# Performance work log

Measured on AMD Instinct MI355X. Metric: run time of the kernel, lower is better.

The kernel has to match this reference:

```python
import jax, jax.numpy as jnp
import numpy as np

S, B, D, H, FF, L, V, O = 512, 32, 512, 8, 2048, 6, 32000, 1000
DH = D // H
EPS = 1e-5


def layer_norm(x, g, b):
    mu = jnp.mean(x, axis=-1, keepdims=True)
    var = jnp.mean((x - mu) ** 2, axis=-1, keepdims=True)
    return (x - mu) * jax.lax.rsqrt(var + EPS) * g + b


def positional_encoding(seq_len, dim):
    pos = np.arange(seq_len, dtype=np.float32)[:, None]
    i = np.arange(dim)
    angle = pos / (10000.0 ** ((i // 2 * 2.0) / dim))
    pe = np.where(i % 2 == 0, np.sin(angle), np.cos(angle)).astype(np.float32)
    return jnp.asarray(pe)  # [seq_len, dim]


def setup_inputs() -> dict:
    key = jax.random.key(0)
    ks = jax.random.split(key, 16)
    sc = 0.02
    inp = {
        'x': jax.random.randint(ks[0], (S, B), 0, V, dtype=jnp.int32),
        'x_len': jnp.full((B,), S, dtype=jnp.int32),
        'emb': jax.random.normal(ks[1], (V, D), jnp.float32) * sc,
        'Wq': jax.random.normal(ks[2], (L, D, D), jnp.float32) * sc,
        'bq': jnp.zeros((L, D), jnp.float32),
        'Wk': jax.random.normal(ks[3], (L, D, D), jnp.float32) * sc,
        'bk': jnp.zeros((L, D), jnp.float32),
        'Wv': jax.random.normal(ks[4], (L, D, D), jnp.float32) * sc,
        'bv': jnp.zeros((L, D), jnp.float32),
        'Wo': jax.random.normal(ks[5], (L, D, D), jnp.float32) * sc,
        'bo': jnp.zeros((L, D), jnp.float32),
        'ln1_g': jnp.ones((L, D), jnp.float32),
        'ln1_b': jnp.zeros((L, D), jnp.float32),
        'W1': jax.random.normal(ks[6], (L, D, FF), jnp.float32) * sc,
        'b1': jnp.zeros((L, FF), jnp.float32),
        'W2': jax.random.normal(ks[7], (L, FF, D), jnp.float32) * sc,
        'b2': jnp.zeros((L, D), jnp.float32),
        'ln2_g': jnp.ones((L, D), jnp.float32),
        'ln2_b': jnp.zeros((L, D), jnp.float32),
        'W_fc': jax.random.normal(ks[8], (S * D, O), jnp.float32) * sc,
        'b_fc': jnp.zeros((O,), jnp.float32),
    }
    return inp


def reference(x, x_len, emb, Wq, bq, Wk, bk, Wv, bv, Wo, bo, ln1_g, ln1_b,
              W1, b1, W2, b2, ln2_g, ln2_b, W_fc, b_fc):
    out = emb[x]                      # [S, B, D]
    out = jnp.transpose(out, (1, 0, 2))  # [B, S, D]
    out = out + positional_encoding(S, D)[None, :, :]
    scale = DH ** -0.5
    for l in range(L):
        # NOTE: faithful to the original buggy head-split: plain row-major
        # reshape [B,S,D] -> [B*H,S,DH] without a [B,H,S,DH] transpose.
        q = jnp.reshape(out @ Wq[l] + bq[l], (B * H, S, DH))
        k = jnp.reshape(out @ Wk[l] + bk[l], (B * H, S, DH))
        v = jnp.reshape(out @ Wv[l] + bv[l], (B * H, S, DH))
        attn = jax.nn.softmax(jnp.einsum('gqd,gkd->gqk', q, k) * scale, axis=-1)
        ctx = jnp.einsum('gqk,gkd->gqd', attn, v).reshape(B, S, D)
        h = layer_norm(ctx @ Wo[l] + bo[l] + out, ln1_g[l], ln1_b[l])
        f = jax.nn.relu(h @ W1[l] + b1[l]) @ W2[l] + b2[l]
        out = layer_norm(f + h, ln2_g[l], ln2_b[l])
    out = out.reshape(B, S * D)
    return out @ W_fc + b_fc          # [B, O]
```

## Files before the change

kernel.cpp:

```cpp
#include <hip/hip_runtime.h>
#include <cstdint>
#include <cstddef>

#define S_  512
#define B_  32
#define D_  512
#define FF_ 2048
#define L_  6
#define O_  1000
#define M_  (B_*S_)
#define G_  256
#define DH_ 64

typedef __attribute__((ext_vector_type(8))) short bf16x8;
typedef __attribute__((ext_vector_type(4))) float f32x4;
typedef __attribute__((ext_vector_type(16))) float f32x16;

__device__ __forceinline__ unsigned short f2bf(float f) {
  unsigned int u = __builtin_bit_cast(unsigned int, f);
  u = (u + 0x7fffu + ((u >> 16) & 1u)) >> 16;
  return (unsigned short)u;
}
__device__ __forceinline__ float bf2f(unsigned short u) {
  return __builtin_bit_cast(float, (unsigned int)u << 16);
}
__device__ __forceinline__ unsigned int pkbf(float a, float b) {
  return (unsigned int)f2bf(a) | ((unsigned int)f2bf(b) << 16);
}
__device__ __forceinline__ void gload_lds16(const void* g, void* l) {
  __builtin_amdgcn_global_load_lds(
      (const __attribute__((address_space(1))) unsigned int*)g,
      (__attribute__((address_space(3))) unsigned int*)l, 16, 0, 0);
}

__global__ void pe_kernel(float* __restrict__ pe) {
  int i = blockIdx.x * 256 + threadIdx.x;
  int s = i >> 9, d = i & 511;
  double de = (double)(d & ~1);
  double ang = (double)s * exp(de * (-9.210340371976184 / 512.0));
  pe[i] = (d & 1) ? (float)cos(ang) : (float)sin(ang);
}

__global__ void wconv_kernel(const float* __restrict__ W, unsigned short* __restrict__ Wt,
                             int K, int N, size_t ozs) {
  __shared__ float tile[32][33];
  const float* Wl = W + (size_t)blockIdx.z * K * N;
  unsigned short* Wtl = Wt + (size_t)blockIdx.z * ozs;
  int k0 = blockIdx.x * 32, n0 = blockIdx.y * 32;
  int c = threadIdx.x & 31, rb = threadIdx.x >> 5;
#pragma unroll
  for (int i = 0; i < 4; ++i) {
    int r = rb + i * 8;
    tile[r][c] = Wl[(size_t)(k0 + r) * N + n0 + c];
  }
  __syncthreads();
#pragma unroll
  for (int i = 0; i < 4; ++i) {
    int r = rb + i * 8;
    Wtl[(size_t)(n0 + r) * K + k0 + c] = f2bf(tile[c][r]);
  }
}

__global__ void embed_kernel(const int* __restrict__ x, const float* __restrict__ emb,
                             const float* __restrict__ pe, unsigned short* __restrict__ xb) {
  int bi = blockIdx.x;
  int s = bi / B_, b = bi % B_;
  int tok = x[s * B_ + b];
  int d = threadIdx.x * 4;
  float4 e = *(const float4*)(emb + (size_t)tok * D_ + d);
  float4 p = *(const float4*)(pe + (size_t)s * D_ + d);
  size_t o = ((size_t)b * S_ + s) * D_ + d;
  ushort4 u;
  u.x = f2bf(e.x + p.x); u.y = f2bf(e.y + p.y);
  u.z = f2bf(e.z + p.z); u.w = f2bf(e.w + p.w);
  *(ushort4*)(xb + o) = u;
}

__global__ __launch_bounds__(256) void gemm_kernel(
    const unsigned short* __restrict__ A, const unsigned short* __restrict__ Bt,
    const float* __restrict__ b0, const float* __restrict__ b1, const float* __restrict__ b2,
    unsigned short* __restrict__ o0, unsigned short* __restrict__ o1, unsigned short* __restrict__ o2,
    int K, int N, int relu, int split, int nbx) {
  __shared__ unsigned short As[3][128 * 32];
  __shared__ unsigned short Bs[3][128 * 32];
  int nwg = nbx * (M_ / 128);
  int cpx = nwg >> 3;
  int id = blockIdx.x;
  int wg = (id % 8) * cpx + id / 8;
  int bx = wg % nbx, by = wg / nbx;
  int m0 = by * 128, n0 = bx * 128;

  int tid = threadIdx.x, lane = tid & 63, wid = tid >> 6;
  int wm = wid >> 1, wn = wid & 1;
  f32x4 acc[4][4];
#pragma unroll
  for (int mi = 0; mi < 4; ++mi)
#pragma unroll
    for (int ni = 0; ni < 4; ++ni) acc[mi][ni] = (f32x4)0.0f;

  int srow = lane >> 2, scol = (lane & 3) * 8;
  const unsigned short* Abase = A + (size_t)m0 * K;
  const unsigned short* Bbase = Bt + (size_t)n0 * K;
  int c16 = lane & 15, hi = lane >> 4;
  int koff = hi * 8;
  int arow = wm * 64 + c16, brow = wn * 64 + c16;
  int nk = K >> 5;

  auto STAGE = [&](int kt, int bb) {
    int k0 = kt * 32;
#pragma unroll
    for (int i = 0; i < 2; ++i) {
      int c = wid * 2 + i;
      gload_lds16(Abase + (size_t)(c * 16 + srow) * K + k0 + scol, (char*)As[bb] + c * 1024);
      gload_lds16(Bbase + (size_t)(c * 16 + srow) * K + k0 + scol, (char*)Bs[bb] + c * 1024);
    }
  };

  STAGE(0, 0); STAGE(1, 1); STAGE(2, 2);
  int bb = 0;
  for (int kt = 0; kt < nk; ++kt) {
    int rem = nk - 1 - kt;
    if (rem >= 2)      asm volatile("s_waitcnt vmcnt(8)" ::: "memory");
    else if (rem == 1) asm volatile("s_waitcnt vmcnt(4)" ::: "memory");
    else               asm volatile("s_waitcnt vmcnt(0)" ::: "memory");
    __builtin_amdgcn_s_barrier();
    __builtin_amdgcn_sched_barrier(0);
    bf16x8 af[4], bfr[4];
#pragma unroll
    for (int mi = 0; mi < 4; ++mi) af[mi] = *(const bf16x8*)&As[bb][(arow + mi * 16) * 32 + koff];
#pragma unroll
    for (int ni = 0; ni < 4; ++ni) bfr[ni] = *(const bf16x8*)&Bs[bb][(brow + ni * 16) * 32 + koff];
    __builtin_amdgcn_s_setprio(1);
#pragma unroll
    for (int mi = 0; mi < 4; ++mi)
#pragma unroll
      for (int ni = 0; ni < 4; ++ni)
        acc[mi][ni] = __builtin_amdgcn_mfma_f32_16x16x32_bf16(bfr[ni], af[mi], acc[mi][ni], 0, 0, 0);
    __builtin_amdgcn_s_setprio(0);
    __builtin_amdgcn_sched_barrier(0);
    __builtin_amdgcn_s_barrier();
    if (kt + 3 < nk) STAGE(kt + 3, bb);
    bb = (bb == 2) ? 0 : bb + 1;
  }

  const float* bias = b0;
  unsigned short* outb = o0;
  int nbase = n0, ostride = N;
  if (split) {
    int seg = n0 >> 9;
    if (seg == 1) { bias = b1; outb = o1; }
    else if (seg == 2) { bias = b2; outb = o2; }
    nbase = n0 & 511; ostride = 512;
  }
#pragma unroll
  for (int ni = 0; ni < 4; ++ni) {
    int colb = nbase + wn * 64 + ni * 16 + hi * 4;
    float4 bv = *(const float4*)(bias + colb);
#pragma unroll
    for (int mi = 0; mi < 4; ++mi) {
      int row = m0 + wm * 64 + mi * 16 + c16;
      float v0 = acc[mi][ni][0] + bv.x;
      float v1 = acc[mi][ni][1] + bv.y;
      float v2 = acc[mi][ni][2] + bv.z;
      float v3 = acc[mi][ni][3] + bv.w;
      if (relu) { v0 = fmaxf(v0, 0.f); v1 = fmaxf(v1, 0.f); v2 = fmaxf(v2, 0.f); v3 = fmaxf(v3, 0.f); }
      *(uint2*)(outb + (size_t)row * ostride + colb) = make_uint2(pkbf(v0, v1), pkbf(v2, v3));
    }
  }
}

__global__ __launch_bounds__(512) void gemmln_kernel(
    const unsigned short* __restrict__ A, const unsigned short* __restrict__ Bt,
    const float* __restrict__ bias, const unsigned short* __restrict__ resid,
    const float* __restrict__ g, const float* __restrict__ bvec,
    unsigned short* __restrict__ Yb, int K) {
  __shared__ unsigned short As[32 * 32];
  __shared__ unsigned short Bs[512 * 32];
  __shared__ float redS[8][32];
  __shared__ float redQ[8][32];
  int tid = threadIdx.x, lane = tid & 63, wid = tid >> 6;
  int wn = wid;
  int m0 = blockIdx.x * 32;
  f32x4 acc[2][4];
#pragma unroll
  for (int mi = 0; mi < 2; ++mi)
#pragma unroll
    for (int ni = 0; ni < 4; ++ni) acc[mi][ni] = (f32x4)0.0f;

  int srow = lane >> 2, scol = (lane & 3) * 8;
  int c16 = lane & 15, hi = lane >> 4;
  int koff = hi * 8;
  int nk = K >> 5;
  for (int kt = 0; kt < nk; ++kt) {
    int k0 = kt * 32;
#pragma unroll
    for (int i = 0; i < 4; ++i) {
      int c = wid * 4 + i;
      gload_lds16(Bt + (size_t)(c * 16 + srow) * K + k0 + scol, (char*)Bs + c * 1024);
    }
    if (wid < 2)
      gload_lds16(A + (size_t)(m0 + wid * 16 + srow) * K + k0 + scol, (char*)As + wid * 1024);
    __syncthreads();
    bf16x8 af[2], bfr[4];
#pragma unroll
    for (int mi = 0; mi < 2; ++mi) af[mi] = *(const bf16x8*)&As[(mi * 16 + c16) * 32 + koff];
#pragma unroll
    for (int ni = 0; ni < 4; ++ni) bfr[ni] = *(const bf16x8*)&Bs[(wn * 64 + ni * 16 + c16) * 32 + koff];
#pragma unroll
    for (int mi = 0; mi < 2; ++mi)
#pragma unroll
      for (int ni = 0; ni < 4; ++ni)
        acc[mi][ni] = __builtin_amdgcn_mfma_f32_16x16x32_bf16(bfr[ni], af[mi], acc[mi][ni], 0, 0, 0);
    __syncthreads();
  }

#pragma unroll
  for (int ni = 0; ni < 4; ++ni) {
    int colb = wn * 64 + ni * 16 + hi * 4;
    float4 bv = *(const float4*)(bias + colb);
#pragma unroll
    for (int mi = 0; mi < 2; ++mi) {
      int row = m0 + mi * 16 + c16;
      ushort4 rv = *(const ushort4*)(resid + (size_t)row * 512 + colb);
      acc[mi][ni][0] += bv.x + bf2f(rv.x);
      acc[mi][ni][1] += bv.y + bf2f(rv.y);
      acc[mi][ni][2] += bv.z + bf2f(rv.z);
      acc[mi][ni][3] += bv.w + bf2f(rv.w);
    }
  }
  float mean_[2], rstd_[2];
#pragma unroll
  for (int mi = 0; mi < 2; ++mi) {
    float s = 0.0f;
#pragma unroll
    for (int ni = 0; ni < 4; ++ni)
#pragma unroll
      for (int r = 0; r < 4; ++r) s += acc[mi][ni][r];
    s += __shfl_xor(s, 16);
    s += __shfl_xor(s, 32);
    if (lane < 16) redS[wn][mi * 16 + lane] = s;
  }
  __syncthreads();
#pragma unroll
  for (int mi = 0; mi < 2; ++mi) {
    int rl = mi * 16 + c16;
    float s = 0.0f;
#pragma unroll
    for (int w = 0; w < 8; ++w) s += redS[w][rl];
    mean_[mi] = s * (1.0f / 512.0f);
  }
#pragma unroll
  for (int mi = 0; mi < 2; ++mi) {
    float ss = 0.0f;
#pragma unroll
    for (int ni = 0; ni < 4; ++ni)
#pragma unroll
      for (int r = 0; r < 4; ++r) {
        float d = acc[mi][ni][r] - mean_[mi];
        ss += d * d;
      }
    ss += __shfl_xor(ss, 16);
    ss += __shfl_xor(ss, 32);
    if (lane < 16) redQ[wn][mi * 16 + lane] = ss;
  }
  __syncthreads();
#pragma unroll
  for (int mi = 0; mi < 2; ++mi) {
    int rl = mi * 16 + c16;
    float ss = 0.0f;
#pragma unroll
    for (int w = 0; w < 8; ++w) ss += redQ[w][rl];
    rstd_[mi] = rsqrtf(ss * (1.0f / 512.0f) + 1e-5f);
  }
#pragma unroll
  for (int mi = 0; mi < 2; ++mi) {
    float mu = mean_[mi], rs = rstd_[mi];
    int row = m0 + mi * 16 + c16;
#pragma unroll
    for (int ni = 0; ni < 4; ++ni) {
      int colb = wn * 64 + ni * 16 + hi * 4;
      float4 gg = *(const float4*)(g + colb);
      float4 bb = *(const float4*)(bvec + colb);
      float y0 = (acc[mi][ni][0] - mu) * rs * gg.x + bb.x;
      float y1 = (acc[mi][ni][1] - mu) * rs * gg.y + bb.y;
      float y2 = (acc[mi][ni][2] - mu) * rs * gg.z + bb.z;
      float y3 = (acc[mi][ni][3] - mu) * rs * gg.w + bb.w;
      *(uint2*)(Yb + (size_t)row * 512 + colb) = make_uint2(pkbf(y0, y1), pkbf(y2, y3));
    }
  }
}

__global__ __launch_bounds__(256) void attn_kernel(
    const unsigned short* __restrict__ Q, const unsigned short* __restrict__ Kb,
    const unsigned short* __restrict__ Vb, unsigned short* __restrict__ Ctx) {
  __shared__ char KlB[8192];
  __shared__ char VtB[8192];
  int g = blockIdx.y;
  int q0 = blockIdx.x * 128;
  const unsigned short* Kg = Kb + (size_t)g * 512 * 64;
  const unsigned short* Vg = Vb + (size_t)g * 512 * 64;
  int tid = threadIdx.x, lane = tid & 63, wid = tid >> 6;
  int l31 = lane & 31, h = lane >> 5;
  bool lo = (lane < 32);
  int qrow = q0 + wid * 32 + l31;
  const float sc2 = 0.125f * 1.44269504f;

  bf16x8 qf[4];
  {
    const unsigned short* qp = Q + ((size_t)g * 512 + qrow) * 64;
#pragma unroll
    for (int c = 0; c < 4; ++c) {
      bf16x8 raw = *(const bf16x8*)(qp + c * 16 + h * 8);
      union { unsigned int u[4]; bf16x8 v; } uu;
#pragma unroll
      for (int j = 0; j < 4; ++j)
        uu.u[j] = pkbf(bf2f((unsigned short)raw[2 * j]) * sc2,
                       bf2f((unsigned short)raw[2 * j + 1]) * sc2);
      qf[c] = uu.v;
    }
  }

  f32x16 c0 = (f32x16)0.0f, c1 = (f32x16)0.0f;
  float mr = -3.0e38f, ls = 0.0f;

  for (int kt = 0; kt < 8; ++kt) {
    __syncthreads();
    {
      int row = tid >> 2;
      size_t base = (size_t)(kt * 64 + row) * 64;
#pragma unroll
      for (int i = 0; i < 2; ++i) {
        int cb = ((tid & 3) + 4 * i) * 16;
        bf16x8 kv = *(const bf16x8*)(Kg + base + cb / 2);
        *(bf16x8*)(KlB + row * 128 + (cb ^ ((row & 7) << 4))) = kv;
        bf16x8 vv = *(const bf16x8*)(Vg + base + cb / 2);
#pragma unroll
        for (int j = 0; j < 8; ++j) {
          int d = cb / 2 + j;
          *(unsigned short*)(VtB + d * 128 + ((2 * row) ^ ((d & 7) << 4))) =
              (unsigned short)vv[j];
        }
      }
    }
    __syncthreads();

    f32x16 s0 = (f32x16)0.0f, s1 = (f32x16)0.0f;
#pragma unroll
    for (int c = 0; c < 4; ++c) {
      int cb = 32 * c + 16 * h;
      int sw = cb ^ ((l31 & 7) << 4);
      bf16x8 k0 = *(const bf16x8*)(KlB + l31 * 128 + sw);
      bf16x8 k1 = *(const bf16x8*)(KlB + (32 + l31) * 128 + sw);
      s0 = __builtin_amdgcn_mfma_f32_32x32x16_bf16(k0, qf[c], s0, 0, 0, 0);
      s1 = __builtin_amdgcn_mfma_f32_32x32x16_bf16(k1, qf[c], s1, 0, 0, 0);
    }

    float pm = s0[0];
#pragma unroll
    for (int i = 1; i < 16; ++i) pm = fmaxf(pm, s0[i]);
#pragma unroll
    for (int i = 0; i < 16; ++i) pm = fmaxf(pm, s1[i]);
    pm = fmaxf(pm, __shfl_xor(pm, 32));
    float mnew = fmaxf(mr, pm);
    float alpha = exp2f(mr - mnew);
    mr = mnew;
    float p[32];
    float rs = 0.0f;
#pragma unroll
    for (int i = 0; i < 16; ++i) { p[i] = exp2f(s0[i] - mnew); rs += p[i]; }
#pragma unroll
    for (int i = 0; i < 16; ++i) { p[16 + i] = exp2f(s1[i] - mnew); rs += p[16 + i]; }
    float rso = __shfl_xor(rs, 32);
    ls = ls * alpha + rs + rso;
#pragma unroll
    for (int i = 0; i < 16; ++i) { c0[i] *= alpha; c1[i] *= alpha; }

    union { unsigned int u[4]; bf16x8 v; } pa[4];
#pragma unroll
    for (int t = 0; t < 2; ++t) {
#pragma unroll
      for (int u = 0; u < 2; ++u) {
#pragma unroll
        for (int pr = 0; pr < 2; ++pr) {
          const int b0i = t * 16 + 8 * u;
          unsigned int a  = pkbf(p[b0i + 2 * pr],     p[b0i + 2 * pr + 1]);
          unsigned int b  = pkbf(p[b0i + 4 + 2 * pr], p[b0i + 4 + 2 * pr + 1]);
          unsigned int sa = __shfl_xor(a, 32);
          unsigned int sb = __shfl_xor(b, 32);
          pa[t * 2 + u].u[pr]     = lo ? a  : sb;
          pa[t * 2 + u].u[2 + pr] = lo ? sa : b;
        }
      }
    }

#pragma unroll
    for (int kc = 0; kc < 4; ++kc) {
      int cb = 32 * kc + 16 * h;
      int sw = cb ^ ((l31 & 7) << 4);
      bf16x8 v0 = *(const bf16x8*)(VtB + l31 * 128 + sw);
      bf16x8 v1 = *(const bf16x8*)(VtB + (32 + l31) * 128 + sw);
      c0 = __builtin_amdgcn_mfma_f32_32x32x16_bf16(v0, pa[kc].v, c0, 0, 0, 0);
      c1 = __builtin_amdgcn_mfma_f32_32x32x16_bf16(v1, pa[kc].v, c1, 0, 0, 0);
    }
  }

  float inv = 1.0f / ls;
  unsigned short* cp = Ctx + ((size_t)g * 512 + qrow) * 64;
#pragma unroll
  for (int dh = 0; dh < 2; ++dh) {
#pragma unroll
    for (int rq = 0; rq < 4; ++rq) {
      float e0 = (dh ? c1[rq * 4 + 0] : c0[rq * 4 + 0]) * inv;
      float e1 = (dh ? c1[rq * 4 + 1] : c0[rq * 4 + 1]) * inv;
      float e2 = (dh ? c1[rq * 4 + 2] : c0[rq * 4 + 2]) * inv;
      float e3 = (dh ? c1[rq * 4 + 3] : c0[rq * 4 + 3]) * inv;
      int d0 = dh * 32 + rq * 8 + h * 4;
      *(uint2*)(cp + d0) = make_uint2(pkbf(e0, e1), pkbf(e2, e3));
    }
  }
}

#define KCH 1024
__global__ __launch_bounds__(256) void fc_part_kernel(const unsigned short* __restrict__ act,
                                                      const float* __restrict__ Wfc,
                                                      float* __restrict__ part) {
  __shared__ float al[32][256];
  int o = blockIdx.x * 256 + threadIdx.x;
  int kc = blockIdx.y;
  size_t k0 = (size_t)kc * KCH;
  float acc[32];
#pragma unroll
  for (int bb = 0; bb < 32; ++bb) acc[bb] = 0.0f;
  for (int sub = 0; sub < KCH / 256; ++sub) {
    __syncthreads();
    for (int i = threadIdx.x; i < 32 * 128; i += 256) {
      int bb = i >> 7, kk = (i & 127) * 2;
      ushort2 u = *(const ushort2*)(act + (size_t)bb * 262144 + k0 + sub * 256 + kk);
      al[bb][kk] = bf2f(u.x);
      al[bb][kk + 1] = bf2f(u.y);
    }
    __syncthreads();
    if (o < O_) {
      const float* wp = Wfc + (k0 + sub * 256) * O_ + o;
      for (int kk = 0; kk < 256; ++kk) {
        float w = wp[(size_t)kk * O_];
#pragma unroll
        for (int bb = 0; bb < 32; ++bb) acc[bb] = fmaf(al[bb][kk], w, acc[bb]);
      }
    }
  }
  if (o < O_) {
#pragma unroll
    for (int bb = 0; bb < 32; ++bb) part[((size_t)kc * 32 + bb) * O_ + o] = acc[bb];
  }
}

__global__ void fc_reduce_kernel(const float* __restrict__ part, const float* __restrict__ bfc,
                                 float* __restrict__ out) {
  int o = blockIdx.x * 256 + threadIdx.x;
  int b = blockIdx.y;
  if (o >= O_) return;
  float s = bfc[o];
  for (int c = 0; c < 256; ++c) s += part[((size_t)c * 32 + b) * O_ + o];
  out[(size_t)b * O_ + o] = s;
}

extern "C" void kernel_launch(void* const* d_in, const int* in_sizes, int n_in,
                              void* d_out, int out_size, void* d_ws, size_t ws_size,
                              hipStream_t stream) {
  const int*   x   = (const int*)d_in[0];
  const float* emb = (const float*)d_in[2];
  const float* Wq  = (const float*)d_in[3];
  const float* bq  = (const float*)d_in[4];
  const float* Wk  = (const float*)d_in[5];
  const float* bk  = (const float*)d_in[6];
  const float* Wv  = (const float*)d_in[7];
  const float* bv  = (const float*)d_in[8];
  const float* Wo  = (const float*)d_in[9];
  const float* bo  = (const float*)d_in[10];
  const float* g1  = (const float*)d_in[11];
  const float* bn1 = (const float*)d_in[12];
  const float* W1  = (const float*)d_in[13];
  const float* bf1 = (const float*)d_in[14];
  const float* W2  = (const float*)d_in[15];
  const float* bf2 = (const float*)d_in[16];
  const float* g2  = (const float*)d_in[17];
  const float* bn2 = (const float*)d_in[18];
  const float* Wfc = (const float*)d_in[19];
  const float* bfc = (const float*)d_in[20];
  float* out = (float*)d_out;

  char* ws = (char*)d_ws;
  size_t off = 0;
  auto take = [&](size_t bytes) { char* p = ws + off; off += (bytes + 255) & ~(size_t)255; return p; };
  float*          pe   = (float*)take((size_t)512 * 512 * 4);
  unsigned short* wqkv = (unsigned short*)take((size_t)L_ * 1536 * 512 * 2);
  unsigned short* wot  = (unsigned short*)take((size_t)L_ * 512 * 512 * 2);
  unsigned short* w1t  = (unsigned short*)take((size_t)L_ * 2048 * 512 * 2);
  unsigned short* w2t  = (unsigned short*)take((size_t)L_ * 512 * 2048 * 2);
  unsigned short* xb   = (unsigned short*)take((size_t)M_ * 512 * 2);
  unsigned short* qb   = (unsigned short*)take((size_t)M_ * 512 * 2);
  unsigned short* kb   = (unsigned short*)take((size_t)M_ * 512 * 2);
  unsigned short* vb   = (unsigned short*)take((size_t)M_ * 512 * 2);
  unsigned short* cxb  = (unsigned short*)take((size_t)M_ * 512 * 2);
  unsigned short* hb   = (unsigned short*)take((size_t)M_ * 512 * 2);
  unsigned short* f1b  = qb;
  float*          part = (float*)qb;

  pe_kernel<<<1024, 256, 0, stream>>>(pe);
  wconv_kernel<<<dim3(16, 16, L_), 256, 0, stream>>>(Wq, wqkv,          512, 512,  (size_t)1536 * 512);
  wconv_kernel<<<dim3(16, 16, L_), 256, 0, stream>>>(Wk, wqkv + 262144, 512, 512,  (size_t)1536 * 512);
  wconv_kernel<<<dim3(16, 16, L_), 256, 0, stream>>>(Wv, wqkv + 524288, 512, 512,  (size_t)1536 * 512);
  wconv_kernel<<<dim3(16, 16, L_), 256, 0, stream>>>(Wo, wot,           512, 512,  (size_t)512 * 512);
  wconv_kernel<<<dim3(16, 64, L_), 256, 0, stream>>>(W1, w1t,           512, 2048, (size_t)2048 * 512);
  wconv_kernel<<<dim3(64, 16, L_), 256, 0, stream>>>(W2, w2t,           2048, 512, (size_t)512 * 2048);
  embed_kernel<<<M_, 128, 0, stream>>>(x, emb, pe, xb);

  for (int l = 0; l < L_; ++l) {
    gemm_kernel<<<12 * 128, 256, 0, stream>>>(
        xb, wqkv + (size_t)l * 1536 * 512,
        bq + l * 512, bk + l * 512, bv + l * 512,
        qb, kb, vb, 512, 1536, 0, 1, 12);
    attn_kernel<<<dim3(4, G_), 256, 0, stream>>>(qb, kb, vb, cxb);
    gemmln_kernel<<<512, 512, 0, stream>>>(
        cxb, wot + (size_t)l * 512 * 512, bo + l * 512, xb,
        g1 + l * 512, bn1 + l * 512, hb, 512);
    gemm_kernel<<<16 * 128, 256, 0, stream>>>(
        hb, w1t + (size_t)l * 2048 * 512,
        bf1 + l * 2048, nullptr, nullptr,
        f1b, nullptr, nullptr, 512, 2048, 1, 0, 16);
    gemmln_kernel<<<512, 512, 0, stream>>>(
        f1b, w2t + (size_t)l * 512 * 2048, bf2 + l * 512, hb,
        g2 + l * 512, bn2 + l * 512, xb, 2048);
  }

  fc_part_kernel<<<dim3(4, 256), 256, 0, stream>>>(xb, Wfc, part);
  fc_reduce_kernel<<<dim3(4, 32), 256, 0, stream>>>(part, bfc, out);
}
```

Before: 2.189 ms.

## Widen GEMM tile to 128x256 and split fused GEMM+LayerNorm into GEMM plus add-LN

The main GEMM kernel now uses 512 threads and a 128x256 output tile, so each workgroup loads its A tile once for twice as many columns. The unpipelined fused GEMM+LayerNorm kernels, which used 32-row tiles and reloaded the whole weight matrix per block, are replaced by the pipelined wide GEMM writing a bf16 intermediate, followed by a separate add-residual LayerNorm kernel. This should raise MFMA efficiency for the Wo and W2 projections at the cost of an extra activation round trip through memory and an extra bf16 rounding before the LayerNorm. Only 256 workgroups are launched for the N=512 GEMMs, which may underfill the device.

```diff
diff --git a/kernel.cpp b/kernel.cpp
--- a/kernel.cpp
+++ b/kernel.cpp
@@ -76,22 +76,22 @@
   *(ushort4*)(xb + o) = u;
 }
 
-__global__ __launch_bounds__(256) void gemm_kernel(
+__global__ __launch_bounds__(512) void gemm_kernel(
     const unsigned short* __restrict__ A, const unsigned short* __restrict__ Bt,
     const float* __restrict__ b0, const float* __restrict__ b1, const float* __restrict__ b2,
     unsigned short* __restrict__ o0, unsigned short* __restrict__ o1, unsigned short* __restrict__ o2,
     int K, int N, int relu, int split, int nbx) {
   __shared__ unsigned short As[3][128 * 32];
-  __shared__ unsigned short Bs[3][128 * 32];
+  __shared__ unsigned short Bs[3][256 * 32];
   int nwg = nbx * (M_ / 128);
   int cpx = nwg >> 3;
   int id = blockIdx.x;
   int wg = (id % 8) * cpx + id / 8;
   int bx = wg % nbx, by = wg / nbx;
-  int m0 = by * 128, n0 = bx * 128;
+  int m0 = by * 128, n0 = bx * 256;
 
   int tid = threadIdx.x, lane = tid & 63, wid = tid >> 6;
-  int wm = wid >> 1, wn = wid & 1;
+  int wm = wid >> 2, wn = wid & 3;
   f32x4 acc[4][4];
 #pragma unroll
   for (int mi = 0; mi < 4; ++mi)
@@ -108,10 +108,10 @@
 
   auto STAGE = [&](int kt, int bb) {
     int k0 = kt * 32;
+    gload_lds16(Abase + (size_t)(wid * 16 + srow) * K + k0 + scol, (char*)As[bb] + wid * 1024);
 #pragma unroll
     for (int i = 0; i < 2; ++i) {
       int c = wid * 2 + i;
-      gload_lds16(Abase + (size_t)(c * 16 + srow) * K + k0 + scol, (char*)As[bb] + c * 1024);
       gload_lds16(Bbase + (size_t)(c * 16 + srow) * K + k0 + scol, (char*)Bs[bb] + c * 1024);
     }
   };
@@ -120,8 +120,8 @@
   int bb = 0;
   for (int kt = 0; kt < nk; ++kt) {
     int rem = nk - 1 - kt;
-    if (rem >= 2)      asm volatile("s_waitcnt vmcnt(8)" ::: "memory");
-    else if (rem == 1) asm volatile("s_waitcnt vmcnt(4)" ::: "memory");
+    if (rem >= 2)      asm volatile("s_waitcnt vmcnt(6)" ::: "memory");
+    else if (rem == 1) asm volatile("s_waitcnt vmcnt(3)" ::: "memory");
     else               asm volatile("s_waitcnt vmcnt(0)" ::: "memory");
     __builtin_amdgcn_s_barrier();
     __builtin_amdgcn_sched_barrier(0);
@@ -169,125 +169,40 @@
   }
 }
 
-__global__ __launch_bounds__(512) void gemmln_kernel(
-    const unsigned short* __restrict__ A, const unsigned short* __restrict__ Bt,
-    const float* __restrict__ bias, const unsigned short* __restrict__ resid,
-    const float* __restrict__ g, const float* __restrict__ bvec,
-    unsigned short* __restrict__ Yb, int K) {
-  __shared__ unsigned short As[32 * 32];
-  __shared__ unsigned short Bs[512 * 32];
-  __shared__ float redS[8][32];
-  __shared__ float redQ[8][32];
-  int tid = threadIdx.x, lane = tid & 63, wid = tid >> 6;
-  int wn = wid;
-  int m0 = blockIdx.x * 32;
-  f32x4 acc[2][4];
-#pragma unroll
-  for (int mi = 0; mi < 2; ++mi)
-#pragma unroll
-    for (int ni = 0; ni < 4; ++ni) acc[mi][ni] = (f32x4)0.0f;
-
-  int srow = lane >> 2, scol = (lane & 3) * 8;
-  int c16 = lane & 15, hi = lane >> 4;
-  int koff = hi * 8;
-  int nk = K >> 5;
-  for (int kt = 0; kt < nk; ++kt) {
-    int k0 = kt * 32;
-#pragma unroll
-    for (int i = 0; i < 4; ++i) {
-      int c = wid * 4 + i;
-      gload_lds16(Bt + (size_t)(c * 16 + srow) * K + k0 + scol, (char*)Bs + c * 1024);
-    }
-    if (wid < 2)
-      gload_lds16(A + (size_t)(m0 + wid * 16 + srow) * K + k0 + scol, (char*)As + wid * 1024);
-    __syncthreads();
-    bf16x8 af[2], bfr[4];
-#pragma unroll
-    for (int mi = 0; mi < 2; ++mi) af[mi] = *(const bf16x8*)&As[(mi * 16 + c16) * 32 + koff];
-#pragma unroll
-    for (int ni = 0; ni < 4; ++ni) bfr[ni] = *(const bf16x8*)&Bs[(wn * 64 + ni * 16 + c16) * 32 + koff];
-#pragma unroll
-    for (int mi = 0; mi < 2; ++mi)
-#pragma unroll
-      for (int ni = 0; ni < 4; ++ni)
-        acc[mi][ni] = __builtin_amdgcn_mfma_f32_16x16x32_bf16(bfr[ni], af[mi], acc[mi][ni], 0, 0, 0);
-    __syncthreads();
-  }
-
-#pragma unroll
-  for (int ni = 0; ni < 4; ++ni) {
-    int colb = wn * 64 + ni * 16 + hi * 4;
-    float4 bv = *(const float4*)(bias + colb);
-#pragma unroll
-    for (int mi = 0; mi < 2; ++mi) {
-      int row = m0 + mi * 16 + c16;
-      ushort4 rv = *(const ushort4*)(resid + (size_t)row * 512 + colb);
-      acc[mi][ni][0] += bv.x + bf2f(rv.x);
-      acc[mi][ni][1] += bv.y + bf2f(rv.y);
-      acc[mi][ni][2] += bv.z + bf2f(rv.z);
-      acc[mi][ni][3] += bv.w + bf2f(rv.w);
-    }
-  }
-  float mean_[2], rstd_[2];
-#pragma unroll
-  for (int mi = 0; mi < 2; ++mi) {
-    float s = 0.0f;
-#pragma unroll
-    for (int ni = 0; ni < 4; ++ni)
-#pragma unroll
-      for (int r = 0; r < 4; ++r) s += acc[mi][ni][r];
-    s += __shfl_xor(s, 16);
-    s += __shfl_xor(s, 32);
-    if (lane < 16) redS[wn][mi * 16 + lane] = s;
-  }
+__global__ __launch_bounds__(128) void addln_kernel(
+    const unsigned short* __restrict__ Y, const unsigned short* __restrict__ R,
+    const float* __restrict__ g, const float* __restrict__ b,
+    unsigned short* __restrict__ Out) {
+  __shared__ float red[2], red2[2];
+  int row = blockIdx.x, t = threadIdx.x;
+  size_t o = (size_t)row * 512 + t * 4;
+  ushort4 yv = *(const ushort4*)(Y + o);
+  ushort4 rv = *(const ushort4*)(R + o);
+  float v0 = bf2f(yv.x) + bf2f(rv.x);
+  float v1 = bf2f(yv.y) + bf2f(rv.y);
+  float v2 = bf2f(yv.z) + bf2f(rv.z);
+  float v3 = bf2f(yv.w) + bf2f(rv.w);
+  float s = v0 + v1 + v2 + v3;
+#pragma unroll
+  for (int m = 1; m < 64; m <<= 1) s += __shfl_xor(s, m);
+  if ((t & 63) == 0) red[t >> 6] = s;
   __syncthreads();
-#pragma unroll
-  for (int mi = 0; mi < 2; ++mi) {
-    int rl = mi * 16 + c16;
-    float s = 0.0f;
-#pragma unroll
-    for (int w = 0; w < 8; ++w) s += redS[w][rl];
-    mean_[mi] = s * (1.0f / 512.0f);
-  }
-#pragma unroll
-  for (int mi = 0; mi < 2; ++mi) {
-    float ss = 0.0f;
-#pragma unroll
-    for (int ni = 0; ni < 4; ++ni)
-#pragma unroll
-      for (int r = 0; r < 4; ++r) {
-        float d = acc[mi][ni][r] - mean_[mi];
-        ss += d * d;
-      }
-    ss += __shfl_xor(ss, 16);
-    ss += __shfl_xor(ss, 32);
-    if (lane < 16) redQ[wn][mi * 16 + lane] = ss;
-  }
+  float mean = (red[0] + red[1]) * (1.0f / 512.0f);
+  float d0 = v0 - mean, d1 = v1 - mean, d2 = v2 - mean, d3 = v3 - mean;
+  float sq = d0 * d0 + d1 * d1 + d2 * d2 + d3 * d3;
+#pragma unroll
+  for (int m = 1; m < 64; m <<= 1) sq += __shfl_xor(sq, m);
+  if ((t & 63) == 0) red2[t >> 6] = sq;
   __syncthreads();
-#pragma unroll
-  for (int mi = 0; mi < 2; ++mi) {
-    int rl = mi * 16 + c16;
-    float ss = 0.0f;
-#pragma unroll
-    for (int w = 0; w < 8; ++w) ss += redQ[w][rl];
-    rstd_[mi] = rsqrtf(ss * (1.0f / 512.0f) + 1e-5f);
-  }
-#pragma unroll
-  for (int mi = 0; mi < 2; ++mi) {
-    float mu = mean_[mi], rs = rstd_[mi];
-    int row = m0 + mi * 16 + c16;
-#pragma unroll
-    for (int ni = 0; ni < 4; ++ni) {
-      int colb = wn * 64 + ni * 16 + hi * 4;
-      float4 gg = *(const float4*)(g + colb);
-      float4 bb = *(const float4*)(bvec + colb);
-      float y0 = (acc[mi][ni][0] - mu) * rs * gg.x + bb.x;
-      float y1 = (acc[mi][ni][1] - mu) * rs * gg.y + bb.y;
-      float y2 = (acc[mi][ni][2] - mu) * rs * gg.z + bb.z;
-      float y3 = (acc[mi][ni][3] - mu) * rs * gg.w + bb.w;
-      *(uint2*)(Yb + (size_t)row * 512 + colb) = make_uint2(pkbf(y0, y1), pkbf(y2, y3));
-    }
-  }
+  float var = (red2[0] + red2[1]) * (1.0f / 512.0f);
+  float rstd = rsqrtf(var + 1e-5f);
+  float4 gg = *(const float4*)(g + t * 4);
+  float4 bb = *(const float4*)(b + t * 4);
+  float y0 = d0 * rstd * gg.x + bb.x;
+  float y1 = d1 * rstd * gg.y + bb.y;
+  float y2 = d2 * rstd * gg.z + bb.z;
+  float y3 = d3 * rstd * gg.w + bb.w;
+  *(uint2*)(Out + o) = make_uint2(pkbf(y0, y1), pkbf(y2, y3));
 }
 
 __global__ __launch_bounds__(256) void attn_kernel(
@@ -504,6 +419,7 @@
   unsigned short* vb   = (unsigned short*)take((size_t)M_ * 512 * 2);
   unsigned short* cxb  = (unsigned short*)take((size_t)M_ * 512 * 2);
   unsigned short* hb   = (unsigned short*)take((size_t)M_ * 512 * 2);
+  unsigned short* t1   = (unsigned short*)take((size_t)M_ * 512 * 2);
   unsigned short* f1b  = qb;
   float*          part = (float*)qb;
 
@@ -517,21 +433,25 @@
   embed_kernel<<<M_, 128, 0, stream>>>(x, emb, pe, xb);
 
   for (int l = 0; l < L_; ++l) {
-    gemm_kernel<<<12 * 128, 256, 0, stream>>>(
+    gemm_kernel<<<768, 512, 0, stream>>>(
         xb, wqkv + (size_t)l * 1536 * 512,
         bq + l * 512, bk + l * 512, bv + l * 512,
-        qb, kb, vb, 512, 1536, 0, 1, 12);
+        qb, kb, vb, 512, 1536, 0, 1, 6);
     attn_kernel<<<dim3(4, G_), 256, 0, stream>>>(qb, kb, vb, cxb);
-    gemmln_kernel<<<512, 512, 0, stream>>>(
-        cxb, wot + (size_t)l * 512 * 512, bo + l * 512, xb,
-        g1 + l * 512, bn1 + l * 512, hb, 512);
-    gemm_kernel<<<16 * 128, 256, 0, stream>>>(
+    gemm_kernel<<<256, 512, 0, stream>>>(
+        cxb, wot + (size_t)l * 512 * 512,
+        bo + l * 512, nullptr, nullptr,
+        t1, nullptr, nullptr, 512, 512, 0, 0, 2);
+    addln_kernel<<<M_, 128, 0, stream>>>(t1, xb, g1 + l * 512, bn1 + l * 512, hb);
+    gemm_kernel<<<1024, 512, 0, stream>>>(
         hb, w1t + (size_t)l * 2048 * 512,
         bf1 + l * 2048, nullptr, nullptr,
-        f1b, nullptr, nullptr, 512, 2048, 1, 0, 16);
-    gemmln_kernel<<<512, 512, 0, stream>>>(
-        f1b, w2t + (size_t)l * 512 * 2048, bf2 + l * 512, hb,
-        g2 + l * 512, bn2 + l * 512, xb, 2048);
+        f1b, nullptr, nullptr, 512, 2048, 1, 0, 8);
+    gemm_kernel<<<256, 512, 0, stream>>>(
+        f1b, w2t + (size_t)l * 512 * 2048,
+        bf2 + l * 512, nullptr, nullptr,
+        t1, nullptr, nullptr, 2048, 512, 0, 0, 2);
+    addln_kernel<<<M_, 128, 0, stream>>>(t1, hb, g2 + l * 512, bn2 + l * 512, xb);
   }
 
   fc_part_kernel<<<dim3(4, 256), 256, 0, stream>>>(xb, Wfc, part);
```

Result: faster. 2.121 ms (-3.1%).
